# Kernel optimization log

Measured on AMD Instinct MI355X. Metric: run time of the kernel, lower is better.

## Reference

```python
import jax, jax.numpy as jnp
import numpy as np

HEAD_NUM = 16
NEG_BIG = 1e12


def setup_inputs() -> dict:
    key = jax.random.key(0)
    ks = jax.random.split(key, 10)
    B, S, H = 4, 2048, 1024
    std = 0.02
    return {
        "encoder_outputs": jax.random.normal(ks[0], (B, S, H), dtype=jnp.float32),
        "mask": jax.random.randint(ks[1], (B, S), 0, 2, dtype=jnp.int32),
        "Wq": jax.random.normal(ks[2], (H, H), dtype=jnp.float32) * std,
        "bq": jax.random.normal(ks[3], (H,), dtype=jnp.float32) * std,
        "Wk": jax.random.normal(ks[4], (H, H), dtype=jnp.float32) * std,
        "bk": jax.random.normal(ks[5], (H,), dtype=jnp.float32) * std,
        "Wv": jax.random.normal(ks[6], (H, H), dtype=jnp.float32) * std,
        "bv": jax.random.normal(ks[7], (H,), dtype=jnp.float32) * std,
        "Wc": jax.random.normal(ks[8], (H, H), dtype=jnp.float32) * std,
    }


def _split_heads(x, h):
    # chunk(h, -1) + stack(dim=0): [B,S,H] -> [h,B,S,H//h]
    B, S, H = x.shape
    return jnp.moveaxis(x.reshape(B, S, h, H // h), 2, 0)


def reference(encoder_outputs, mask, Wq, bq, Wk, bk, Wv, bv, Wc):
    x = encoder_outputs
    B, S, H = x.shape
    hd = H // HEAD_NUM
    q = _split_heads(x @ Wq.T + bq, HEAD_NUM)  # [h,B,S,hd]
    k = _split_heads(x @ Wk.T + bk, HEAD_NUM)
    v = _split_heads(x @ Wv.T + bv, HEAD_NUM)
    dots = jnp.einsum("hbqd,hbkd->hbqk", q, k) / jnp.sqrt(jnp.float32(hd))
    m = mask.astype(jnp.float32)  # [B,S]; 0 = valid token
    inv = 1.0 - m
    eye = jnp.eye(S, dtype=jnp.float32)
    # clamp_max(1 - (1-m)_i (1-m)_j + eye, 1): [B,S,S]
    new_mask = jnp.minimum(1.0 - inv[:, :, None] * inv[:, None, :] + eye, 1.0)
    energies = dots - new_mask[None] * NEG_BIG
    weights = jax.nn.softmax(energies, axis=-1) * (1.0 - new_mask)[None]
    out = jnp.einsum("hbqk,hbkd->hbqd", weights, v)  # [h,B,S,hd]
    out = jnp.moveaxis(out, 0, 2).reshape(B, S, H)  # concat heads
    return out @ Wc.T
```

## Files before the change

kernel.cpp:

```cpp
#include <hip/hip_runtime.h>
#include <cstddef>
#include <cstdint>

#define BB 4
#define SS 2048
#define HH 1024
#define NH 16
#define HD 64

typedef _Float16 half8 __attribute__((ext_vector_type(8)));
typedef _Float16 half4v __attribute__((ext_vector_type(4)));
typedef float f32x4 __attribute__((ext_vector_type(4)));

#define KSCALE 0.1803368801111f

__device__ __forceinline__ void gload_lds16(const _Float16* g, char* l) {
    __builtin_amdgcn_global_load_lds(
        (const __attribute__((address_space(1))) void*)g,
        (__attribute__((address_space(3))) void*)l, 16, 0, 0);
}

__global__ __launch_bounds__(256)
void scan_mask(const int* __restrict__ mk, int* __restrict__ vidx, int* __restrict__ cnt)
{
    __shared__ int ps[256];
    const int b = blockIdx.x, t = threadIdx.x;
    int flag[8], s = 0;
#pragma unroll
    for (int k = 0; k < 8; ++k) { flag[k] = (mk[(b << 11) + t * 8 + k] == 0); s += flag[k]; }
    ps[t] = s;
    __syncthreads();
    for (int off = 1; off < 256; off <<= 1) {
        const int add = (t >= off) ? ps[t - off] : 0;
        __syncthreads();
        ps[t] += add;
        __syncthreads();
    }
    int pos = ps[t] - s;
#pragma unroll
    for (int k = 0; k < 8; ++k)
        if (flag[k]) vidx[(b << 11) + pos++] = t * 8 + k;
    if (t == 255) cnt[b] = ps[255];
}

__global__ __launch_bounds__(256)
void gather_x(const float* __restrict__ x, const int* __restrict__ vidx,
              const int* __restrict__ cnt, _Float16* __restrict__ xc)
{
    const int row = blockIdx.x;
    const int b = row >> 11, i = row & 2047;
    const int t = threadIdx.x;
    half4v hv = (half4v){0, 0, 0, 0};
    if (i < cnt[b]) {
        const float4 v = ((const float4*)(x + (size_t)((b << 11) + vidx[row]) * HH))[t];
        hv[0] = (_Float16)v.x; hv[1] = (_Float16)v.y;
        hv[2] = (_Float16)v.z; hv[3] = (_Float16)v.w;
    }
    ((half4v*)(xc + (size_t)row * HH))[t] = hv;
}

__global__ __launch_bounds__(256)
void cvt_w(const float* __restrict__ Wq, const float* __restrict__ Wk,
           const float* __restrict__ Wv, const float* __restrict__ Wc,
           _Float16* __restrict__ o)
{
    const float* src = blockIdx.z == 0 ? Wq : blockIdx.z == 1 ? Wk :
                       blockIdx.z == 2 ? Wv : Wc;
    _Float16* dst = o + (size_t)blockIdx.z * (HH * HH);
    const int i = blockIdx.x * 256 + threadIdx.x;
    const float4 v0 = ((const float4*)src)[(size_t)i * 2];
    const float4 v1 = ((const float4*)src)[(size_t)i * 2 + 1];
    half8 hv;
    hv[0] = (_Float16)v0.x; hv[1] = (_Float16)v0.y;
    hv[2] = (_Float16)v0.z; hv[3] = (_Float16)v0.w;
    hv[4] = (_Float16)v1.x; hv[5] = (_Float16)v1.y;
    hv[6] = (_Float16)v1.z; hv[7] = (_Float16)v1.w;
    ((half8*)dst)[i] = hv;
}

__device__ __forceinline__ void gemm_core(const _Float16* __restrict__ A,
                                          const _Float16* __restrict__ W,
                                          int K, int m0, int n0,
                                          char* As, char* Bs, f32x4 acc[4][4])
{
    const int t = threadIdx.x;
    const int w = t >> 6, lane = t & 63;
    const int ln = lane & 15, g = lane >> 4;
    const int wr = w >> 1, wc = w & 1;

    const int rr0 = w * 16 + (lane >> 2);
    const int rr1 = rr0 + 64;
    const int p   = lane & 3;
    const int sl0 = p ^ ((rr0 >> 1) & 3);
    const int sl1 = p ^ ((rr1 >> 1) & 3);
    const _Float16* ga0 = A + (size_t)(m0 + rr0) * K + sl0 * 8;
    const _Float16* ga1 = A + (size_t)(m0 + rr1) * K + sl1 * 8;
    const _Float16* gb0 = W + (size_t)(n0 + rr0) * K + sl0 * 8;
    const _Float16* gb1 = W + (size_t)(n0 + rr1) * K + sl1 * 8;
    char* dA = As + w * 1024 + lane * 16;
    char* dB = Bs + w * 1024 + lane * 16;

    int offA[4], offB[4];
#pragma unroll
    for (int i = 0; i < 4; ++i) {
        const int ra = wr * 64 + i * 16 + ln;
        offA[i] = ra * 64 + ((g ^ ((ra >> 1) & 3)) << 4);
        const int rb = wc * 64 + i * 16 + ln;
        offB[i] = rb * 64 + ((g ^ ((rb >> 1) & 3)) << 4);
    }

#pragma unroll
    for (int i = 0; i < 4; ++i)
#pragma unroll
        for (int j = 0; j < 4; ++j) acc[i][j] = (f32x4){0.f, 0.f, 0.f, 0.f};

    gload_lds16(ga0, dA);
    gload_lds16(ga1, dA + 4096);
    gload_lds16(gb0, dB);
    gload_lds16(gb1, dB + 4096);
    gload_lds16(ga0 + 32, dA + 8192);
    gload_lds16(ga1 + 32, dA + 8192 + 4096);
    gload_lds16(gb0 + 32, dB + 8192);
    gload_lds16(gb1 + 32, dB + 8192 + 4096);

    const int ns = K / 32;
    for (int k = 0; k < ns; ++k) {
        if (k < ns - 1) { asm volatile("s_waitcnt vmcnt(4)" ::: "memory"); }
        else            { asm volatile("s_waitcnt vmcnt(0)" ::: "memory"); }
        __builtin_amdgcn_s_barrier();
        __builtin_amdgcn_sched_barrier(0);

        const char* Ab = As + ((k & 1) << 13);
        const char* Bb = Bs + ((k & 1) << 13);
        half8 af[4], bf[4];
#pragma unroll
        for (int i = 0; i < 4; ++i) af[i] = *(const half8*)(Ab + offA[i]);
#pragma unroll
        for (int j = 0; j < 4; ++j) bf[j] = *(const half8*)(Bb + offB[j]);

        asm volatile("s_waitcnt lgkmcnt(0)" ::: "memory");
        __builtin_amdgcn_s_barrier();
        __builtin_amdgcn_sched_barrier(0);

        if (k + 2 < ns) {
            const int nb = (k & 1) << 13;
            const int ko = (k + 2) * 32;
            gload_lds16(ga0 + ko, dA + nb);
            gload_lds16(ga1 + ko, dA + nb + 4096);
            gload_lds16(gb0 + ko, dB + nb);
            gload_lds16(gb1 + ko, dB + nb + 4096);
        }
#pragma unroll
        for (int i = 0; i < 4; ++i)
#pragma unroll
            for (int j = 0; j < 4; ++j)
                acc[i][j] = __builtin_amdgcn_mfma_f32_16x16x32_f16(af[i], bf[j], acc[i][j], 0, 0, 0);
    }
}

__global__ __launch_bounds__(256)
void gemm_qkv(const _Float16* __restrict__ xc,
              const _Float16* __restrict__ Wq16, const _Float16* __restrict__ Wk16,
              const _Float16* __restrict__ Wv16,
              const float* __restrict__ bq, const float* __restrict__ bk,
              const float* __restrict__ bv, const int* __restrict__ cnt,
              _Float16* __restrict__ Qh, _Float16* __restrict__ Kh,
              _Float16* __restrict__ Vt)
{
    const int m0 = blockIdx.y * 128;
    const int bI = m0 >> 11;
    if ((m0 & 2047) >= ((cnt[bI] + 127) & ~127)) return;

    __shared__ __align__(16) char As[16384];
    __shared__ __align__(16) char Bs[16384];
    const int z = blockIdx.z;
    const _Float16* W = (z == 0) ? Wq16 : (z == 1) ? Wk16 : Wv16;
    const float* bias = (z == 0) ? bq : (z == 1) ? bk : bv;
    const int n0 = blockIdx.x * 128;

    f32x4 acc[4][4];
    gemm_core(xc, W, HH, m0, n0, As, Bs, acc);

    const int t = threadIdx.x;
    const int w = t >> 6, lane = t & 63;
    const int ln = lane & 15, g = lane >> 4;
    const int wr = w >> 1, wc = w & 1;
    const int mBase = m0 + wr * 64 + g * 4;
    const int nBase = n0 + wc * 64 + ln;

    if (z < 2) {
        _Float16* O = z ? Kh : Qh;
        const float sc = z ? 1.0f : KSCALE;
#pragma unroll
        for (int j = 0; j < 4; ++j) {
            const int n = nBase + j * 16;
            const int h = n >> 6, d = n & 63;
            const float bvf = bias[n];
#pragma unroll
            for (int i = 0; i < 4; ++i) {
                const int m = mBase + i * 16;
                const int b = m >> 11, s = m & 2047;
                _Float16* dst = O + (((size_t)(b * NH + h) * SS + s) * HD + d);
#pragma unroll
                for (int r = 0; r < 4; ++r)
                    dst[(size_t)r * HD] = (_Float16)((acc[i][j][r] + bvf) * sc);
            }
        }
    } else {
#pragma unroll
        for (int j = 0; j < 4; ++j) {
            const int n = nBase + j * 16;
            const int h = n >> 6, d = n & 63;
            const float bvf = bias[n];
#pragma unroll
            for (int i = 0; i < 4; ++i) {
                const int m = mBase + i * 16;
                const int b = m >> 11, s = m & 2047;
                const int sp = (s & ~31) | (((s >> 2) & 3) << 3) | (((s >> 4) & 1) << 2);
                half4v v;
#pragma unroll
                for (int r = 0; r < 4; ++r) v[r] = (_Float16)(acc[i][j][r] + bvf);
                *(half4v*)(Vt + ((size_t)(b * NH + h) * HD + d) * SS + sp) = v;
            }
        }
    }
}

__global__ __launch_bounds__(256)
void gemm_out(const _Float16* __restrict__ Oc, const _Float16* __restrict__ Wc16,
              const int* __restrict__ cnt, const int* __restrict__ vidx,
              float* __restrict__ C)
{
    const int m0 = blockIdx.y * 128;
    const int bI = m0 >> 11;
    const int cb = cnt[bI];
    if ((m0 & 2047) >= ((cb + 127) & ~127)) return;

    __shared__ __align__(16) char As[16384];
    __shared__ __align__(16) char Bs[16384];
    const int n0 = blockIdx.x * 128;

    f32x4 acc[4][4];
    gemm_core(Oc, Wc16, HH, m0, n0, As, Bs, acc);

    const int t = threadIdx.x;
    const int w = t >> 6, lane = t & 63;
    const int ln = lane & 15, g = lane >> 4;
    const int wr = w >> 1, wc = w & 1;
    const int mBase = m0 + wr * 64 + g * 4;
    const int nBase = n0 + wc * 64 + ln;
#pragma unroll
    for (int i = 0; i < 4; ++i) {
#pragma unroll
        for (int r = 0; r < 4; ++r) {
            const int m = mBase + i * 16 + r;
            const int lm = m & 2047;
            if (lm < cb) {
                const int orig = vidx[m];
                const size_t off = (size_t)((m & ~2047) + orig) * HH + nBase;
#pragma unroll
                for (int j = 0; j < 4; ++j)
                    C[off + j * 16] = acc[i][j][r];
            }
        }
    }
}

__global__ __launch_bounds__(512, 4)
void attn_mfma(const _Float16* __restrict__ Qh, const _Float16* __restrict__ Kh,
               const _Float16* __restrict__ Vt, const int* __restrict__ cnt,
               _Float16* __restrict__ Oc)
{
    __shared__ __align__(16) char ksm[3][8192];
    __shared__ __align__(16) char vsm[3][8192];

    const int t  = threadIdx.x;
    const int w  = t >> 6, l = t & 63, ln = l & 15, g = l >> 4;
    const int bh = blockIdx.x;
    const int b  = bh >> 4, h = bh & 15;
    const int cb = cnt[b];
    const int q0 = blockIdx.y << 7;
    if (q0 >= cb) return;
    const int qw = q0 + (w << 4);
    const bool active = (qw < cb);
    const int nt = (cb + 63) >> 6;
    const int jtd = qw >> 6;
    const int qoff = qw & 63;

    half8 qf[2];
    f32x4 oacc[4];
    float lrun = 0.f;
    if (active) {
        const int qg = qw + ln;
        const _Float16* qp = Qh + ((size_t)bh * SS + qg) * HD + g * 8;
        qf[0] = *(const half8*)qp;
        qf[1] = *(const half8*)(qp + 32);
#pragma unroll
        for (int dd = 0; dd < 4; ++dd) oacc[dd] = (f32x4){0.f, 0.f, 0.f, 0.f};
    }

    const int sr = t >> 3;
    const int sl = (t & 7) ^ (sr & 7);
    const _Float16* kbase = Kh + ((size_t)bh * SS + sr) * HD + sl * 8;
    const _Float16* vbase = Vt + ((size_t)bh * HD + sr) * SS + sl * 8;

    gload_lds16(kbase, ksm[0] + t * 16);
    gload_lds16(vbase, vsm[0] + t * 16);
    if (nt > 1) {
        gload_lds16(kbase + (size_t)64 * HD, ksm[1] + t * 16);
        gload_lds16(vbase + 64,              vsm[1] + t * 16);
    }

    int cur = 0;
    for (int jt = 0; jt < nt; ++jt) {
        if (jt < nt - 1) { asm volatile("s_waitcnt vmcnt(2) lgkmcnt(0)" ::: "memory"); }
        else             { asm volatile("s_waitcnt vmcnt(0) lgkmcnt(0)" ::: "memory"); }
        __builtin_amdgcn_s_barrier();
        __builtin_amdgcn_sched_barrier(0);

        if (jt + 2 < nt) {
            const int nb = (cur + 2 >= 3) ? cur - 1 : cur + 2;
            const int jn = (jt + 2) << 6;
            gload_lds16(kbase + (size_t)jn * HD, ksm[nb] + t * 16);
            gload_lds16(vbase + jn,              vsm[nb] + t * 16);
        }

        if (active) {
            const int j0 = jt << 6;
            const char* kb = ksm[cur];
            const char* vb = vsm[cur];
            half8 kf[4][2];
#pragma unroll
            for (int tau = 0; tau < 4; ++tau) {
                const int row = tau * 16 + ln;
                const int sw  = (row & 7) << 4;
                const int rb  = row * 128;
                kf[tau][0] = *(const half8*)(kb + ((rb + g * 16)      ^ sw));
                kf[tau][1] = *(const half8*)(kb + ((rb + 64 + g * 16) ^ sw));
            }
            const bool slow = (jt == jtd) | (j0 + 64 > cb);

            f32x4 sa[4];
            __builtin_amdgcn_s_setprio(1);
#pragma unroll
            for (int tau = 0; tau < 4; ++tau) {
                sa[tau] = (f32x4){0.f, 0.f, 0.f, 0.f};
                sa[tau] = __builtin_amdgcn_mfma_f32_16x16x32_f16(kf[tau][0], qf[0], sa[tau], 0, 0, 0);
                sa[tau] = __builtin_amdgcn_mfma_f32_16x16x32_f16(kf[tau][1], qf[1], sa[tau], 0, 0, 0);
            }
            __builtin_amdgcn_s_setprio(0);

            float wv[4][4], rs = 0.f;
#pragma unroll
            for (int tau = 0; tau < 4; ++tau)
#pragma unroll
                for (int r = 0; r < 4; ++r) {
                    float tv = sa[tau][r];
                    if (slow) {
                        const int kp = tau * 16 + g * 4 + r;
                        const int rel = qoff + ln;
                        if (((jt == jtd) & (kp == rel)) | (j0 + kp >= cb))
                            tv = -1e30f;
                    }
                    const float e = exp2f(tv);
                    wv[tau][r] = e; rs += e;
                }
            lrun += rs;

            half8 pf[2];
#pragma unroll
            for (int kk = 0; kk < 2; ++kk) {
                half8 pp;
                pp[0] = (_Float16)wv[2*kk][0];     pp[1] = (_Float16)wv[2*kk][1];
                pp[2] = (_Float16)wv[2*kk][2];     pp[3] = (_Float16)wv[2*kk][3];
                pp[4] = (_Float16)wv[2*kk+1][0];   pp[5] = (_Float16)wv[2*kk+1][1];
                pp[6] = (_Float16)wv[2*kk+1][2];   pp[7] = (_Float16)wv[2*kk+1][3];
                pf[kk] = pp;
            }

            __builtin_amdgcn_s_setprio(1);
#pragma unroll
            for (int dd = 0; dd < 4; ++dd) {
                const int row = dd * 16 + ln;
                const int sw  = (row & 7) << 4;
                const int rb  = row * 128;
#pragma unroll
                for (int kk = 0; kk < 2; ++kk) {
                    const half8 vf = *(const half8*)(vb + ((rb + kk * 64 + g * 16) ^ sw));
                    oacc[dd] = __builtin_amdgcn_mfma_f32_16x16x32_f16(vf, pf[kk], oacc[dd], 0, 0, 0);
                }
            }
            __builtin_amdgcn_s_setprio(0);
        }
        cur = (cur + 1 == 3) ? 0 : cur + 1;
    }

    if (active) {
        float ls = lrun;
        ls += __shfl_xor(ls, 16);
        ls += __shfl_xor(ls, 32);
        const int iq = qw + ln;
        if (iq < cb) {
            const float inv = (ls > 0.f) ? 1.f / ls : 0.f;
            _Float16* op = Oc + ((size_t)((b << 11) + iq)) * HH + h * HD + g * 4;
#pragma unroll
            for (int dd = 0; dd < 4; ++dd) {
                half4v hv;
#pragma unroll
                for (int r = 0; r < 4; ++r) hv[r] = (_Float16)(oacc[dd][r] * inv);
                *(half4v*)(op + dd * 16) = hv;
            }
        }
    }
}

extern "C" void kernel_launch(void* const* d_in, const int* in_sizes, int n_in,
                              void* d_out, int out_size, void* d_ws, size_t ws_size,
                              hipStream_t stream)
{
    (void)in_sizes; (void)n_in; (void)ws_size;

    const float* x  = (const float*)d_in[0];
    const int*   mk = (const int*)d_in[1];
    const float* Wq = (const float*)d_in[2];
    const float* bq = (const float*)d_in[3];
    const float* Wk = (const float*)d_in[4];
    const float* bk = (const float*)d_in[5];
    const float* Wv = (const float*)d_in[6];
    const float* bv = (const float*)d_in[7];
    const float* Wc = (const float*)d_in[8];
    float* out = (float*)d_out;

    const int M = BB * SS;
    const size_t NE = (size_t)M * HH;
    const size_t NW = (size_t)HH * HH;
    _Float16* xc  = (_Float16*)d_ws;
    _Float16* W16 = xc + NE;
    _Float16* Qh  = W16 + 4 * NW;
    _Float16* Kh  = Qh + NE;
    _Float16* Vt  = Kh + NE;
    _Float16* Oc  = Vt + NE;
    int* vidx = (int*)(Oc + NE);
    int* cnt  = vidx + M;

    hipMemsetAsync(out, 0, (size_t)out_size * sizeof(float), stream);
    scan_mask<<<BB, 256, 0, stream>>>(mk, vidx, cnt);
    gather_x<<<M, 256, 0, stream>>>(x, vidx, cnt, xc);
    cvt_w<<<dim3(512, 1, 4), 256, 0, stream>>>(Wq, Wk, Wv, Wc, W16);

    dim3 gq(HH / 128, M / 128, 3);
    gemm_qkv<<<gq, 256, 0, stream>>>(xc, W16, W16 + NW, W16 + 2 * NW,
                                     bq, bk, bv, cnt, Qh, Kh, Vt);

    dim3 ga(BB * NH, SS / 128);
    attn_mfma<<<ga, 512, 0, stream>>>(Qh, Kh, Vt, cnt, Oc);

    dim3 go(HH / 128, M / 128);
    gemm_out<<<go, 256, 0, stream>>>(Oc, W16 + 3 * NW, cnt, vidx, out);
}
```

Baseline: 140.2 us.

## Split each attention key tile across two waves per query group and combine partials

Each block now covers 64 queries instead of 128. Its 8 waves form 4 query groups, with two waves per group that each handle half of every 64-key tile. The partial output accumulators and row sums from the second half are reduced through LDS (reusing the V buffer) before normalisation and store. The intent is to double the number of blocks and halve the per-wave MFMA chain length, giving better occupancy and latency hiding. The cost is twice the K/V tile loads per query across blocks, plus an extra barrier-and-reduce epilogue.

Result: faster. 135.1 us (-3.6%).

```diff
diff --git a/kernel.cpp b/kernel.cpp
--- a/kernel.cpp
+++ b/kernel.cpp
@@ -279,13 +279,15 @@
     const int bh = blockIdx.x;
     const int b  = bh >> 4, h = bh & 15;
     const int cb = cnt[b];
-    const int q0 = blockIdx.y << 7;
+    const int q0 = blockIdx.y << 6;
     if (q0 >= cb) return;
-    const int qw = q0 + (w << 4);
+    const int p  = w & 3;
+    const int hf = w >> 2;
+    const int qw = q0 + (p << 4);
     const bool active = (qw < cb);
     const int nt = (cb + 63) >> 6;
     const int jtd = qw >> 6;
-    const int qoff = qw & 63;
+    const int rel = (qw & 63) + ln;
 
     half8 qf[2];
     f32x4 oacc[4];
@@ -329,54 +331,48 @@
             const int j0 = jt << 6;
             const char* kb = ksm[cur];
             const char* vb = vsm[cur];
-            half8 kf[4][2];
-#pragma unroll
-            for (int tau = 0; tau < 4; ++tau) {
-                const int row = tau * 16 + ln;
+            half8 kf[2][2];
+#pragma unroll
+            for (int tu = 0; tu < 2; ++tu) {
+                const int row = (hf * 2 + tu) * 16 + ln;
                 const int sw  = (row & 7) << 4;
                 const int rb  = row * 128;
-                kf[tau][0] = *(const half8*)(kb + ((rb + g * 16)      ^ sw));
-                kf[tau][1] = *(const half8*)(kb + ((rb + 64 + g * 16) ^ sw));
+                kf[tu][0] = *(const half8*)(kb + ((rb + g * 16)      ^ sw));
+                kf[tu][1] = *(const half8*)(kb + ((rb + 64 + g * 16) ^ sw));
             }
             const bool slow = (jt == jtd) | (j0 + 64 > cb);
 
-            f32x4 sa[4];
+            f32x4 sa[2];
             __builtin_amdgcn_s_setprio(1);
 #pragma unroll
-            for (int tau = 0; tau < 4; ++tau) {
-                sa[tau] = (f32x4){0.f, 0.f, 0.f, 0.f};
-                sa[tau] = __builtin_amdgcn_mfma_f32_16x16x32_f16(kf[tau][0], qf[0], sa[tau], 0, 0, 0);
-                sa[tau] = __builtin_amdgcn_mfma_f32_16x16x32_f16(kf[tau][1], qf[1], sa[tau], 0, 0, 0);
+            for (int tu = 0; tu < 2; ++tu) {
+                sa[tu] = (f32x4){0.f, 0.f, 0.f, 0.f};
+                sa[tu] = __builtin_amdgcn_mfma_f32_16x16x32_f16(kf[tu][0], qf[0], sa[tu], 0, 0, 0);
+                sa[tu] = __builtin_amdgcn_mfma_f32_16x16x32_f16(kf[tu][1], qf[1], sa[tu], 0, 0, 0);
             }
             __builtin_amdgcn_s_setprio(0);
 
-            float wv[4][4], rs = 0.f;
-#pragma unroll
-            for (int tau = 0; tau < 4; ++tau)
+            float wv[2][4];
+#pragma unroll
+            for (int tu = 0; tu < 2; ++tu)
 #pragma unroll
                 for (int r = 0; r < 4; ++r) {
-                    float tv = sa[tau][r];
+                    float tv = sa[tu][r];
                     if (slow) {
-                        const int kp = tau * 16 + g * 4 + r;
-                        const int rel = qoff + ln;
+                        const int kp = (hf * 2 + tu) * 16 + g * 4 + r;
                         if (((jt == jtd) & (kp == rel)) | (j0 + kp >= cb))
                             tv = -1e30f;
                     }
-                    const float e = exp2f(tv);
-                    wv[tau][r] = e; rs += e;
+                    wv[tu][r] = exp2f(tv);
                 }
-            lrun += rs;
-
-            half8 pf[2];
-#pragma unroll
-            for (int kk = 0; kk < 2; ++kk) {
-                half8 pp;
-                pp[0] = (_Float16)wv[2*kk][0];     pp[1] = (_Float16)wv[2*kk][1];
-                pp[2] = (_Float16)wv[2*kk][2];     pp[3] = (_Float16)wv[2*kk][3];
-                pp[4] = (_Float16)wv[2*kk+1][0];   pp[5] = (_Float16)wv[2*kk+1][1];
-                pp[6] = (_Float16)wv[2*kk+1][2];   pp[7] = (_Float16)wv[2*kk+1][3];
-                pf[kk] = pp;
-            }
+            lrun += ((wv[0][0] + wv[0][1]) + (wv[0][2] + wv[0][3]))
+                  + ((wv[1][0] + wv[1][1]) + (wv[1][2] + wv[1][3]));
+
+            half8 pf;
+            pf[0] = (_Float16)wv[0][0]; pf[1] = (_Float16)wv[0][1];
+            pf[2] = (_Float16)wv[0][2]; pf[3] = (_Float16)wv[0][3];
+            pf[4] = (_Float16)wv[1][0]; pf[5] = (_Float16)wv[1][1];
+            pf[6] = (_Float16)wv[1][2]; pf[7] = (_Float16)wv[1][3];
 
             __builtin_amdgcn_s_setprio(1);
 #pragma unroll
@@ -384,19 +380,27 @@
                 const int row = dd * 16 + ln;
                 const int sw  = (row & 7) << 4;
                 const int rb  = row * 128;
-#pragma unroll
-                for (int kk = 0; kk < 2; ++kk) {
-                    const half8 vf = *(const half8*)(vb + ((rb + kk * 64 + g * 16) ^ sw));
-                    oacc[dd] = __builtin_amdgcn_mfma_f32_16x16x32_f16(vf, pf[kk], oacc[dd], 0, 0, 0);
-                }
+                const half8 vf = *(const half8*)(vb + ((rb + hf * 64 + g * 16) ^ sw));
+                oacc[dd] = __builtin_amdgcn_mfma_f32_16x16x32_f16(vf, pf, oacc[dd], 0, 0, 0);
             }
             __builtin_amdgcn_s_setprio(0);
         }
         cur = (cur + 1 == 3) ? 0 : cur + 1;
     }
 
-    if (active) {
-        float ls = lrun;
+    __syncthreads();
+    f32x4* cmo = (f32x4*)vsm;
+    float* cml = (float*)(cmo + 1024);
+    if (active && hf == 1) {
+#pragma unroll
+        for (int dd = 0; dd < 4; ++dd) cmo[(p * 4 + dd) * 64 + l] = oacc[dd];
+        cml[p * 64 + l] = lrun;
+    }
+    __syncthreads();
+    if (active && hf == 0) {
+#pragma unroll
+        for (int dd = 0; dd < 4; ++dd) oacc[dd] += cmo[(p * 4 + dd) * 64 + l];
+        float ls = lrun + cml[p * 64 + l];
         ls += __shfl_xor(ls, 16);
         ls += __shfl_xor(ls, 32);
         const int iq = qw + ln;
@@ -452,7 +456,7 @@
     gemm_qkv<<<gq, 256, 0, stream>>>(xc, W16, W16 + NW, W16 + 2 * NW,
                                      bq, bk, bv, cnt, Qh, Kh, Vt);
 
-    dim3 ga(BB * NH, SS / 128);
+    dim3 ga(BB * NH, SS / 64);
     attn_mfma<<<ga, 512, 0, stream>>>(Qh, Kh, Vt, cnt, Oc);
 
     dim3 go(HH / 128, M / 128);
```
